# Kernel optimization log

Measured on AMD Instinct MI355X. Metric: run time of the kernel, lower is better.

## Reference

```python
import jax, jax.numpy as jnp
import numpy as np

NUM_EMBEDDINGS = 1024
EMBEDDING_DIM = 64
BETA = 0.25


def setup_inputs() -> dict:
    key = jax.random.key(0)
    k1, k2 = jax.random.split(key)
    z = jax.random.normal(k1, (16, EMBEDDING_DIM, 64, 64), dtype=jnp.float32)
    # matches torch init: uniform_(-1/K, 1/K)
    lim = 1.0 / NUM_EMBEDDINGS
    embedding = jax.random.uniform(k2, (NUM_EMBEDDINGS, EMBEDDING_DIM),
                                   dtype=jnp.float32, minval=-lim, maxval=lim)
    return {"z": z, "embedding": embedding}


def reference(z, embedding):
    B, C, H, W = z.shape  # C == EMBEDDING_DIM
    # [B,C,H,W] -> [B*H*W, C]
    z_flat = jnp.transpose(z, (0, 2, 3, 1)).reshape(-1, C)
    # squared euclidean distances (argmin-equivalent to torch.cdist):
    # ||z||^2 - 2 z.e + ||e||^2 ; shape [N, K]
    d = (jnp.sum(z_flat * z_flat, axis=-1, keepdims=True)
         - 2.0 * (z_flat @ embedding.T)
         + jnp.sum(embedding * embedding, axis=-1))
    encoding_indices = jnp.argmin(d, axis=1)  # [N] int
    z_q_flat = embedding[encoding_indices]    # gather [N, C]
    z_q = jnp.transpose(z_q_flat.reshape(B, H, W, C), (0, 3, 1, 2))
    vq_loss = jnp.mean(jnp.square(jax.lax.stop_gradient(z_q) - z))
    commitment_loss = BETA * jnp.mean(jnp.square(jax.lax.stop_gradient(z) - z_q))
    return (z_q, encoding_indices, vq_loss + commitment_loss)
```

## Files before the change

### kernel.cpp

```cpp
#include <hip/hip_runtime.h>

#define N_PIX   65536
#define CDIM    64
#define KCODES  1024
#define HWSZ    4096
#define KCHUNK  128
#define NCHUNK  8
#define TPB     256
#define PXT     2
#define GRIDX   (N_PIX / (TPB * PXT))

#define OFF_CTR  0
#define OFF_MIN  1024
#define OFF_IDX  525312
#define OFF_LOSS 1049600

#define OUT_IDX  (N_PIX * CDIM)
#define OUT_LOSS (OUT_IDX + N_PIX)

typedef __attribute__((ext_vector_type(16))) float f32x16;

__device__ __forceinline__ float np_nz(const float* zr) {
    float r0 = zr[0]*zr[0], r1 = zr[1]*zr[1], r2 = zr[2]*zr[2], r3 = zr[3]*zr[3];
    float r4 = zr[4]*zr[4], r5 = zr[5]*zr[5], r6 = zr[6]*zr[6], r7 = zr[7]*zr[7];
#pragma unroll
    for (int i = 8; i < CDIM; i += 8) {
        r0 = r0 + zr[i+0]*zr[i+0]; r1 = r1 + zr[i+1]*zr[i+1];
        r2 = r2 + zr[i+2]*zr[i+2]; r3 = r3 + zr[i+3]*zr[i+3];
        r4 = r4 + zr[i+4]*zr[i+4]; r5 = r5 + zr[i+5]*zr[i+5];
        r6 = r6 + zr[i+6]*zr[i+6]; r7 = r7 + zr[i+7]*zr[i+7];
    }
    return ((r0 + r1) + (r2 + r3)) + ((r4 + r5) + (r6 + r7));
}

__global__ __launch_bounds__(TPB, 3) void vq_argmin(const float* __restrict__ z,
                                                    const float* __restrict__ emb,
                                                    float* __restrict__ cmin,
                                                    int* __restrict__ cidx,
                                                    float* __restrict__ ws) {
#pragma clang fp contract(off)
    __shared__ float se[KCHUNK * CDIM];
    __shared__ float sn[KCHUNK];

    const int chunk = blockIdx.y;
    const int k0 = chunk * KCHUNK;

    if ((blockIdx.x | blockIdx.y) == 0 && threadIdx.x == 0) {
        ws[OFF_LOSS] = 0.0f;
        ((unsigned*)ws)[OFF_CTR] = 0u;
    }

    const float4* esrc = (const float4*)(emb + (size_t)k0 * CDIM);
    float4* edst = (float4*)se;
    for (int i = threadIdx.x; i < KCHUNK * CDIM / 4; i += TPB) edst[i] = esrc[i];
    __syncthreads();
    if (threadIdx.x < KCHUNK) {
        const float* e = se + threadIdx.x * CDIM;
        float r0 = e[0]*e[0], r1 = e[1]*e[1], r2 = e[2]*e[2], r3 = e[3]*e[3];
        float r4 = e[4]*e[4], r5 = e[5]*e[5], r6 = e[6]*e[6], r7 = e[7]*e[7];
#pragma unroll
        for (int i = 8; i < CDIM; i += 8) {
            r0 = r0 + e[i+0]*e[i+0]; r1 = r1 + e[i+1]*e[i+1];
            r2 = r2 + e[i+2]*e[i+2]; r3 = r3 + e[i+3]*e[i+3];
            r4 = r4 + e[i+4]*e[i+4]; r5 = r5 + e[i+5]*e[i+5];
            r6 = r6 + e[i+6]*e[i+6]; r7 = r7 + e[i+7]*e[i+7];
        }
        sn[threadIdx.x] = ((r0 + r1) + (r2 + r3)) + ((r4 + r5) + (r6 + r7));
    }
    __syncthreads();

    const int p0 = blockIdx.x * (TPB * PXT) + threadIdx.x;
    const int p1 = p0 + TPB;

    float zr0[CDIM], zr1[CDIM];
    {
        const int b0  = p0 >> 12, hw0 = p0 & (HWSZ - 1);
        const int b1  = p1 >> 12, hw1 = p1 & (HWSZ - 1);
        const float* zp0 = z + ((size_t)(b0 * CDIM) << 12) + hw0;
        const float* zp1 = z + ((size_t)(b1 * CDIM) << 12) + hw1;
#pragma unroll
        for (int c = 0; c < CDIM; ++c) {
            zr0[c] = zp0[(size_t)c << 12];
            zr1[c] = zp1[(size_t)c << 12];
        }
    }
    const float nz0 = np_nz(zr0);
    const float nz1 = np_nz(zr1);

    float best0 = 3.4e38f, best1 = 3.4e38f;
    int   bi0   = k0,      bi1   = k0;

    for (int kk = 0; kk < KCHUNK; kk += 2) {
        const float* erow = emb + (size_t)(k0 + kk) * CDIM;
        f32x16 ec0, ec1, ec2, ec3;
        asm volatile(
            "s_load_dwordx16 %0, %4, 0x100\n\t"
            "s_load_dwordx16 %1, %4, 0x140\n\t"
            "s_load_dwordx16 %2, %4, 0x180\n\t"
            "s_load_dwordx16 %3, %4, 0x1c0"
            : "=s"(ec0), "=s"(ec1), "=s"(ec2), "=s"(ec3)
            : "s"(erow));

        const float4* e0 = (const float4*)(se + kk * CDIM);
        float a00 = 0.f, a01 = 0.f, a10 = 0.f, a11 = 0.f;
#pragma unroll
        for (int j = 0; j < 16; ++j) {
            float4 v0 = e0[j];
            a00 = fmaf(zr0[4*j+0], v0.x, a00);
            a00 = fmaf(zr0[4*j+1], v0.y, a00);
            a00 = fmaf(zr0[4*j+2], v0.z, a00);
            a00 = fmaf(zr0[4*j+3], v0.w, a00);
            a10 = fmaf(zr1[4*j+0], v0.x, a10);
            a10 = fmaf(zr1[4*j+1], v0.y, a10);
            a10 = fmaf(zr1[4*j+2], v0.z, a10);
            a10 = fmaf(zr1[4*j+3], v0.w, a10);
        }

        asm volatile("s_waitcnt lgkmcnt(0)"
                     : "+s"(ec0), "+s"(ec1), "+s"(ec2), "+s"(ec3),
                       "+v"(a00), "+v"(a10));

#pragma unroll
        for (int j = 0; j < 16; ++j) {
            a01 = fmaf(zr0[j], ec0[j], a01);
            a11 = fmaf(zr1[j], ec0[j], a11);
        }
#pragma unroll
        for (int j = 0; j < 16; ++j) {
            a01 = fmaf(zr0[16+j], ec1[j], a01);
            a11 = fmaf(zr1[16+j], ec1[j], a11);
        }
#pragma unroll
        for (int j = 0; j < 16; ++j) {
            a01 = fmaf(zr0[32+j], ec2[j], a01);
            a11 = fmaf(zr1[32+j], ec2[j], a11);
        }
#pragma unroll
        for (int j = 0; j < 16; ++j) {
            a01 = fmaf(zr0[48+j], ec3[j], a01);
            a11 = fmaf(zr1[48+j], ec3[j], a11);
        }

        float d00 = (nz0 - 2.0f * a00) + sn[kk];
        float d01 = (nz0 - 2.0f * a01) + sn[kk + 1];
        float d10 = (nz1 - 2.0f * a10) + sn[kk];
        float d11 = (nz1 - 2.0f * a11) + sn[kk + 1];
        if (d00 < best0) { best0 = d00; bi0 = k0 + kk; }
        if (d01 < best0) { best0 = d01; bi0 = k0 + kk + 1; }
        if (d10 < best1) { best1 = d10; bi1 = k0 + kk; }
        if (d11 < best1) { best1 = d11; bi1 = k0 + kk + 1; }
    }
    cmin[(p0 << 3) + chunk] = best0;
    cidx[(p0 << 3) + chunk] = bi0;
    cmin[(p1 << 3) + chunk] = best1;
    cidx[(p1 << 3) + chunk] = bi1;
}

__global__ __launch_bounds__(TPB) void vq_finalize(const float* __restrict__ z,
                                                   const float* __restrict__ emb,
                                                   const float* __restrict__ cmin,
                                                   const int* __restrict__ cidx,
                                                   float* __restrict__ out,
                                                   float* __restrict__ ws) {
    const int p = blockIdx.x * TPB + threadIdx.x;

    float best = cmin[p << 3];
    int   bi   = cidx[p << 3];
#pragma unroll
    for (int ch = 1; ch < NCHUNK; ++ch) {
        float m = cmin[(p << 3) + ch];
        if (m < best) { best = m; bi = cidx[(p << 3) + ch]; }
    }

    out[OUT_IDX + p] = (float)bi;

    const float* ev = emb + bi * CDIM;
    const int b  = p >> 12;
    const int hw = p & (HWSZ - 1);
    const float* zp = z + ((size_t)(b * CDIM) << 12) + hw;
    float* zq = out + ((size_t)(b * CDIM) << 12) + hw;

    float ls = 0.0f;
#pragma unroll
    for (int c = 0; c < CDIM; ++c) {
        float e = ev[c];
        float zv = zp[(size_t)c << 12];
        float d = e - zv;
        ls = fmaf(d, d, ls);
        zq[(size_t)c << 12] = e;
    }

#pragma unroll
    for (int off = 32; off > 0; off >>= 1) ls += __shfl_down(ls, off);
    __shared__ float wsum[TPB / 64];
    if ((threadIdx.x & 63) == 0) wsum[threadIdx.x >> 6] = ls;
    __syncthreads();
    if (threadIdx.x == 0) {
        float s = wsum[0] + wsum[1] + wsum[2] + wsum[3];
        float* loss_acc = ws + OFF_LOSS;
        atomicAdd(loss_acc, s);
        __threadfence();
        unsigned* ctr = (unsigned*)ws + OFF_CTR;
        unsigned old = atomicAdd(ctr, 1u);
        if (old == (unsigned)(gridDim.x - 1)) {
            __threadfence();
            float total = atomicAdd(loss_acc, 0.0f);
            out[OUT_LOSS] = total * (1.25f / (float)(N_PIX * CDIM));
        }
    }
}

extern "C" void kernel_launch(void* const* d_in, const int* in_sizes, int n_in,
                              void* d_out, int out_size, void* d_ws, size_t ws_size,
                              hipStream_t stream) {
    const float* z   = (const float*)d_in[0];
    const float* emb = (const float*)d_in[1];
    float* ws   = (float*)d_ws;
    float* out  = (float*)d_out;
    float* cmin = ws + OFF_MIN;
    int*   cidx = (int*)(ws + OFF_IDX);

    vq_argmin<<<dim3(GRIDX, NCHUNK), dim3(TPB), 0, stream>>>(z, emb, cmin, cidx, ws);
    vq_finalize<<<dim3(N_PIX / TPB), dim3(TPB), 0, stream>>>(z, emb, cmin, cidx, out, ws);
}
```

Baseline: 196.0 us.

## Halve codebook chunks, stage only even rows in LDS, vectorize finalize reads

```diff
diff --git a/kernel.cpp b/kernel.cpp
--- a/kernel.cpp
+++ b/kernel.cpp
@@ -4,16 +4,17 @@
 #define CDIM    64
 #define KCODES  1024
 #define HWSZ    4096
-#define KCHUNK  128
-#define NCHUNK  8
+#define KCHUNK  256
+#define NCHUNK  4
 #define TPB     256
 #define PXT     2
 #define GRIDX   (N_PIX / (TPB * PXT))
+#define FB      128
 
 #define OFF_CTR  0
 #define OFF_MIN  1024
-#define OFF_IDX  525312
-#define OFF_LOSS 1049600
+#define OFF_IDX  263168
+#define OFF_LOSS 525312
 
 #define OUT_IDX  (N_PIX * CDIM)
 #define OUT_LOSS (OUT_IDX + N_PIX)
@@ -39,7 +40,7 @@
                                                     int* __restrict__ cidx,
                                                     float* __restrict__ ws) {
 #pragma clang fp contract(off)
-    __shared__ float se[KCHUNK * CDIM];
+    __shared__ float se[(KCHUNK / 2) * CDIM];
     __shared__ float sn[KCHUNK];
 
     const int chunk = blockIdx.y;
@@ -50,12 +51,24 @@
         ((unsigned*)ws)[OFF_CTR] = 0u;
     }
 
-    const float4* esrc = (const float4*)(emb + (size_t)k0 * CDIM);
-    float4* edst = (float4*)se;
-    for (int i = threadIdx.x; i < KCHUNK * CDIM / 4; i += TPB) edst[i] = esrc[i];
-    __syncthreads();
-    if (threadIdx.x < KCHUNK) {
-        const float* e = se + threadIdx.x * CDIM;
+    {
+        const int nf4 = (KCHUNK / 2) * (CDIM / 4);
+        for (int i = threadIdx.x; i < nf4; i += TPB) {
+            const int r  = i >> 4;
+            const int c4 = i & 15;
+            ((float4*)se)[i] =
+                *((const float4*)(emb + (size_t)(k0 + 2 * r) * CDIM) + c4);
+        }
+    }
+    {
+        const int k = threadIdx.x;
+        const float4* ep = (const float4*)(emb + (size_t)(k0 + k) * CDIM);
+        float e[CDIM];
+#pragma unroll
+        for (int j = 0; j < 16; ++j) {
+            float4 v = ep[j];
+            e[4*j+0] = v.x; e[4*j+1] = v.y; e[4*j+2] = v.z; e[4*j+3] = v.w;
+        }
         float r0 = e[0]*e[0], r1 = e[1]*e[1], r2 = e[2]*e[2], r3 = e[3]*e[3];
         float r4 = e[4]*e[4], r5 = e[5]*e[5], r6 = e[6]*e[6], r7 = e[7]*e[7];
 #pragma unroll
@@ -65,7 +78,7 @@
             r4 = r4 + e[i+4]*e[i+4]; r5 = r5 + e[i+5]*e[i+5];
             r6 = r6 + e[i+6]*e[i+6]; r7 = r7 + e[i+7]*e[i+7];
         }
-        sn[threadIdx.x] = ((r0 + r1) + (r2 + r3)) + ((r4 + r5) + (r6 + r7));
+        sn[k] = ((r0 + r1) + (r2 + r3)) + ((r4 + r5) + (r6 + r7));
     }
     __syncthreads();
 
@@ -101,7 +114,7 @@
             : "=s"(ec0), "=s"(ec1), "=s"(ec2), "=s"(ec3)
             : "s"(erow));
 
-        const float4* e0 = (const float4*)(se + kk * CDIM);
+        const float4* e0 = (const float4*)(se + (kk >> 1) * CDIM);
         float a00 = 0.f, a01 = 0.f, a10 = 0.f, a11 = 0.f;
 #pragma unroll
         for (int j = 0; j < 16; ++j) {
@@ -150,31 +163,39 @@
         if (d10 < best1) { best1 = d10; bi1 = k0 + kk; }
         if (d11 < best1) { best1 = d11; bi1 = k0 + kk + 1; }
     }
-    cmin[(p0 << 3) + chunk] = best0;
-    cidx[(p0 << 3) + chunk] = bi0;
-    cmin[(p1 << 3) + chunk] = best1;
-    cidx[(p1 << 3) + chunk] = bi1;
-}
-
-__global__ __launch_bounds__(TPB) void vq_finalize(const float* __restrict__ z,
-                                                   const float* __restrict__ emb,
-                                                   const float* __restrict__ cmin,
-                                                   const int* __restrict__ cidx,
-                                                   float* __restrict__ out,
-                                                   float* __restrict__ ws) {
-    const int p = blockIdx.x * TPB + threadIdx.x;
-
-    float best = cmin[p << 3];
-    int   bi   = cidx[p << 3];
-#pragma unroll
-    for (int ch = 1; ch < NCHUNK; ++ch) {
-        float m = cmin[(p << 3) + ch];
-        if (m < best) { best = m; bi = cidx[(p << 3) + ch]; }
-    }
+    cmin[(p0 << 2) + chunk] = best0;
+    cidx[(p0 << 2) + chunk] = bi0;
+    cmin[(p1 << 2) + chunk] = best1;
+    cidx[(p1 << 2) + chunk] = bi1;
+}
+
+__global__ __launch_bounds__(FB) void vq_finalize(const float* __restrict__ z,
+                                                  const float* __restrict__ emb,
+                                                  const float* __restrict__ cmin,
+                                                  const int* __restrict__ cidx,
+                                                  float* __restrict__ out,
+                                                  float* __restrict__ ws) {
+    const int p = blockIdx.x * FB + threadIdx.x;
+
+    const float4 cm = *(const float4*)(cmin + ((size_t)p << 2));
+    const int4   ci = *(const int4*)(cidx + ((size_t)p << 2));
+    float best = cm.x;  int bi = ci.x;
+    if (cm.y < best) { best = cm.y; bi = ci.y; }
+    if (cm.z < best) { best = cm.z; bi = ci.z; }
+    if (cm.w < best) { best = cm.w; bi = ci.w; }
 
     out[OUT_IDX + p] = (float)bi;
 
-    const float* ev = emb + bi * CDIM;
+    float e[CDIM];
+    {
+        const float4* ev = (const float4*)(emb + (size_t)bi * CDIM);
+#pragma unroll
+        for (int j = 0; j < 16; ++j) {
+            float4 v = ev[j];
+            e[4*j+0] = v.x; e[4*j+1] = v.y; e[4*j+2] = v.z; e[4*j+3] = v.w;
+        }
+    }
+
     const int b  = p >> 12;
     const int hw = p & (HWSZ - 1);
     const float* zp = z + ((size_t)(b * CDIM) << 12) + hw;
@@ -183,20 +204,19 @@
     float ls = 0.0f;
 #pragma unroll
     for (int c = 0; c < CDIM; ++c) {
-        float e = ev[c];
         float zv = zp[(size_t)c << 12];
-        float d = e - zv;
+        float d = e[c] - zv;
         ls = fmaf(d, d, ls);
-        zq[(size_t)c << 12] = e;
+        zq[(size_t)c << 12] = e[c];
     }
 
 #pragma unroll
     for (int off = 32; off > 0; off >>= 1) ls += __shfl_down(ls, off);
-    __shared__ float wsum[TPB / 64];
+    __shared__ float wsum[FB / 64];
     if ((threadIdx.x & 63) == 0) wsum[threadIdx.x >> 6] = ls;
     __syncthreads();
     if (threadIdx.x == 0) {
-        float s = wsum[0] + wsum[1] + wsum[2] + wsum[3];
+        float s = wsum[0] + wsum[1];
         float* loss_acc = ws + OFF_LOSS;
         atomicAdd(loss_acc, s);
         __threadfence();
@@ -221,5 +241,5 @@
     int*   cidx = (int*)(ws + OFF_IDX);
 
     vq_argmin<<<dim3(GRIDX, NCHUNK), dim3(TPB), 0, stream>>>(z, emb, cmin, cidx, ws);
-    vq_finalize<<<dim3(N_PIX / TPB), dim3(TPB), 0, stream>>>(z, emb, cmin, cidx, out, ws);
-}
+    vq_finalize<<<dim3(N_PIX / FB), dim3(FB), 0, stream>>>(z, emb, cmin, cidx, out, ws);
+}
```

Measured after the change: 209.5 us. +6.9%, slower.

## Fuse finalize into argmin via packed atomicMin and last-block reduction

Applied to the files above, without the earlier changes.

```diff
diff --git a/kernel.cpp b/kernel.cpp
--- a/kernel.cpp
+++ b/kernel.cpp
@@ -10,10 +10,10 @@
 #define PXT     2
 #define GRIDX   (N_PIX / (TPB * PXT))
 
-#define OFF_CTR  0
-#define OFF_MIN  1024
-#define OFF_IDX  525312
-#define OFF_LOSS 1049600
+#define OFF_PACKED  0
+#define OFF_COLCTR  131072
+#define OFF_CTR2    131200
+#define OFF_LOSS    131204
 
 #define OUT_IDX  (N_PIX * CDIM)
 #define OUT_LOSS (OUT_IDX + N_PIX)
@@ -33,22 +33,26 @@
     return ((r0 + r1) + (r2 + r3)) + ((r4 + r5) + (r6 + r7));
 }
 
+__global__ void vq_init(float* __restrict__ ws) {
+    const int i = blockIdx.x * blockDim.x + threadIdx.x;
+    ((unsigned long long*)ws)[i] = ~0ull;
+    if (i < GRIDX) ((unsigned*)(ws + OFF_COLCTR))[i] = 0u;
+    if (i == 0) {
+        ((unsigned*)(ws + OFF_CTR2))[0] = 0u;
+        ws[OFF_LOSS] = 0.0f;
+    }
+}
+
 __global__ __launch_bounds__(TPB, 3) void vq_argmin(const float* __restrict__ z,
                                                     const float* __restrict__ emb,
-                                                    float* __restrict__ cmin,
-                                                    int* __restrict__ cidx,
+                                                    float* __restrict__ out,
                                                     float* __restrict__ ws) {
 #pragma clang fp contract(off)
     __shared__ float se[KCHUNK * CDIM];
     __shared__ float sn[KCHUNK];
 
-    const int chunk = blockIdx.y;
+    const int chunk = blockIdx.x;
     const int k0 = chunk * KCHUNK;
-
-    if ((blockIdx.x | blockIdx.y) == 0 && threadIdx.x == 0) {
-        ws[OFF_LOSS] = 0.0f;
-        ((unsigned*)ws)[OFF_CTR] = 0u;
-    }
 
     const float4* esrc = (const float4*)(emb + (size_t)k0 * CDIM);
     float4* edst = (float4*)se;
@@ -69,13 +73,13 @@
     }
     __syncthreads();
 
-    const int p0 = blockIdx.x * (TPB * PXT) + threadIdx.x;
+    const int p0 = blockIdx.y * (TPB * PXT) + threadIdx.x;
     const int p1 = p0 + TPB;
+    const int b0 = p0 >> 12, hw0 = p0 & (HWSZ - 1);
+    const int b1 = p1 >> 12, hw1 = p1 & (HWSZ - 1);
 
     float zr0[CDIM], zr1[CDIM];
     {
-        const int b0  = p0 >> 12, hw0 = p0 & (HWSZ - 1);
-        const int b1  = p1 >> 12, hw1 = p1 & (HWSZ - 1);
         const float* zp0 = z + ((size_t)(b0 * CDIM) << 12) + hw0;
         const float* zp1 = z + ((size_t)(b1 * CDIM) << 12) + hw1;
 #pragma unroll
@@ -150,44 +154,67 @@
         if (d10 < best1) { best1 = d10; bi1 = k0 + kk; }
         if (d11 < best1) { best1 = d11; bi1 = k0 + kk + 1; }
     }
-    cmin[(p0 << 3) + chunk] = best0;
-    cidx[(p0 << 3) + chunk] = bi0;
-    cmin[(p1 << 3) + chunk] = best1;
-    cidx[(p1 << 3) + chunk] = bi1;
-}
-
-__global__ __launch_bounds__(TPB) void vq_finalize(const float* __restrict__ z,
-                                                   const float* __restrict__ emb,
-                                                   const float* __restrict__ cmin,
-                                                   const int* __restrict__ cidx,
-                                                   float* __restrict__ out,
-                                                   float* __restrict__ ws) {
-    const int p = blockIdx.x * TPB + threadIdx.x;
-
-    float best = cmin[p << 3];
-    int   bi   = cidx[p << 3];
-#pragma unroll
-    for (int ch = 1; ch < NCHUNK; ++ch) {
-        float m = cmin[(p << 3) + ch];
-        if (m < best) { best = m; bi = cidx[(p << 3) + ch]; }
-    }
-
-    out[OUT_IDX + p] = (float)bi;
-
-    const float* ev = emb + bi * CDIM;
-    const int b  = p >> 12;
-    const int hw = p & (HWSZ - 1);
-    const float* zp = z + ((size_t)(b * CDIM) << 12) + hw;
-    float* zq = out + ((size_t)(b * CDIM) << 12) + hw;
+
+    unsigned long long* packed = (unsigned long long*)ws;
+    const unsigned long long pk0 =
+        ((unsigned long long)__float_as_uint(best0) << 32) | (unsigned)bi0;
+    const unsigned long long pk1 =
+        ((unsigned long long)__float_as_uint(best1) << 32) | (unsigned)bi1;
+    atomicMin(packed + p0, pk0);
+    atomicMin(packed + p1, pk1);
+    __threadfence();
+
+    __shared__ int lastf;
+    if (threadIdx.x == 0) {
+        unsigned old = atomicAdd((unsigned*)(ws + OFF_COLCTR) + blockIdx.y, 1u);
+        lastf = (old == NCHUNK - 1);
+    }
+    __syncthreads();
+    if (!lastf) return;
+
+    const unsigned long long q0 = atomicAdd(packed + p0, 0ull);
+    const unsigned long long q1 = atomicAdd(packed + p1, 0ull);
+    const int wbi0 = (int)(q0 & 0xFFFFFFFFull);
+    const int wbi1 = (int)(q1 & 0xFFFFFFFFull);
+    out[OUT_IDX + p0] = (float)wbi0;
+    out[OUT_IDX + p1] = (float)wbi1;
 
     float ls = 0.0f;
-#pragma unroll
-    for (int c = 0; c < CDIM; ++c) {
-        float e = ev[c];
-        float zv = zp[(size_t)c << 12];
-        float d = e - zv;
-        ls = fmaf(d, d, ls);
-        zq[(size_t)c << 12] = e;
+    {
+        const float4* ev = (const float4*)(emb + (size_t)wbi0 * CDIM);
+        float* zq = out + ((size_t)(b0 * CDIM) << 12) + hw0;
+        float l = 0.0f;
+#pragma unroll
+        for (int j = 0; j < 16; ++j) {
+            float4 v = ev[j];
+            float d0 = v.x - zr0[4*j+0]; l = fmaf(d0, d0, l);
+            float d1 = v.y - zr0[4*j+1]; l = fmaf(d1, d1, l);
+            float d2 = v.z - zr0[4*j+2]; l = fmaf(d2, d2, l);
+            float d3 = v.w - zr0[4*j+3]; l = fmaf(d3, d3, l);
+            zq[(size_t)(4*j+0) << 12] = v.x;
+            zq[(size_t)(4*j+1) << 12] = v.y;
+            zq[(size_t)(4*j+2) << 12] = v.z;
+            zq[(size_t)(4*j+3) << 12] = v.w;
+        }
+        ls += l;
+    }
+    {
+        const float4* ev = (const float4*)(emb + (size_t)wbi1 * CDIM);
+        float* zq = out + ((size_t)(b1 * CDIM) << 12) + hw1;
+        float l = 0.0f;
+#pragma unroll
+        for (int j = 0; j < 16; ++j) {
+            float4 v = ev[j];
+            float d0 = v.x - zr1[4*j+0]; l = fmaf(d0, d0, l);
+            float d1 = v.y - zr1[4*j+1]; l = fmaf(d1, d1, l);
+            float d2 = v.z - zr1[4*j+2]; l = fmaf(d2, d2, l);
+            float d3 = v.w - zr1[4*j+3]; l = fmaf(d3, d3, l);
+            zq[(size_t)(4*j+0) << 12] = v.x;
+            zq[(size_t)(4*j+1) << 12] = v.y;
+            zq[(size_t)(4*j+2) << 12] = v.z;
+            zq[(size_t)(4*j+3) << 12] = v.w;
+        }
+        ls += l;
     }
 
 #pragma unroll
@@ -196,13 +223,13 @@
     if ((threadIdx.x & 63) == 0) wsum[threadIdx.x >> 6] = ls;
     __syncthreads();
     if (threadIdx.x == 0) {
-        float s = wsum[0] + wsum[1] + wsum[2] + wsum[3];
+        float s = (wsum[0] + wsum[1]) + (wsum[2] + wsum[3]);
         float* loss_acc = ws + OFF_LOSS;
         atomicAdd(loss_acc, s);
         __threadfence();
-        unsigned* ctr = (unsigned*)ws + OFF_CTR;
-        unsigned old = atomicAdd(ctr, 1u);
-        if (old == (unsigned)(gridDim.x - 1)) {
+        unsigned* ctr2 = (unsigned*)(ws + OFF_CTR2);
+        unsigned old = atomicAdd(ctr2, 1u);
+        if (old == (unsigned)(GRIDX - 1)) {
             __threadfence();
             float total = atomicAdd(loss_acc, 0.0f);
             out[OUT_LOSS] = total * (1.25f / (float)(N_PIX * CDIM));
@@ -217,9 +244,7 @@
     const float* emb = (const float*)d_in[1];
     float* ws   = (float*)d_ws;
     float* out  = (float*)d_out;
-    float* cmin = ws + OFF_MIN;
-    int*   cidx = (int*)(ws + OFF_IDX);
-
-    vq_argmin<<<dim3(GRIDX, NCHUNK), dim3(TPB), 0, stream>>>(z, emb, cmin, cidx, ws);
-    vq_finalize<<<dim3(N_PIX / TPB), dim3(TPB), 0, stream>>>(z, emb, cmin, cidx, out, ws);
-}
+
+    vq_init<<<dim3(N_PIX / TPB), dim3(TPB), 0, stream>>>(ws);
+    vq_argmin<<<dim3(NCHUNK, GRIDX), dim3(TPB), 0, stream>>>(z, emb, out, ws);
+}
```

Result: slower. 281.6 us (+43.7%).
